# Optimization experiments

Hardware: AMD Instinct MI355X
Metric: run time of the kernel (lower is better)

## Reference

```python
import jax, jax.numpy as jnp
import numpy as np


def _pairwise_sq_dist(x, y):
    # x: [B, N, 3], y: [B, M, 3] -> P: [B, N, M] squared Euclidean distances
    xx = jnp.sum(x * x, axis=-1)                      # [B, N]
    yy = jnp.sum(y * y, axis=-1)                      # [B, M]
    zz = jnp.einsum('bnd,bmd->bnm', x, y)             # [B, N, M]
    return xx[:, :, None] + yy[:, None, :] - 2.0 * zz


def setup_inputs() -> dict:
    key = jax.random.key(0)
    k1, k2 = jax.random.split(key)
    B, K = 8, 8192
    adv_pc = jax.random.normal(k1, (B, K, 3), dtype=jnp.float32)
    ori_pc = jax.random.normal(k2, (B, K, 3), dtype=jnp.float32)
    weights = jnp.ones((B,), dtype=jnp.float32)
    return {"adv_pc": adv_pc, "ori_pc": ori_pc, "weights": weights}


def reference(adv_pc, ori_pc, weights):
    # P = pairwise_dist(gts=ori_pc, preds=adv_pc): [B, N_ori, N_adv]
    P = _pairwise_sq_dist(ori_pc, adv_pc)
    # method='adv2ori': loss1 = max over adv points of min over ori points
    loss1 = jnp.max(jnp.min(P, axis=1), axis=1)       # [B]
    loss = loss1 * weights
    return jnp.mean(loss)                             # batch_avg=True
```

## Files before the change

### kernel.cpp

```cpp
#include <hip/hip_runtime.h>


#define KPTS 8192
#define BATCH 8
#define NSPLIT 8
#define RBLK (KPTS / NSPLIT)
#define TSLICE (RBLK / 32)
#define CBLK 512
#define MCHUNK (KPTS / CBLK)
#define AHALF_B (KPTS * 16)

typedef _Float16 half8 __attribute__((ext_vector_type(8)));
typedef float f32x16 __attribute__((ext_vector_type(16)));

__device__ __forceinline__ float min16acc(float rm, const f32x16 c) {
    float u0 = fminf(fminf(c[0],  c[1]),  c[2]);
    float u1 = fminf(fminf(c[3],  c[4]),  c[5]);
    float u2 = fminf(fminf(c[6],  c[7]),  c[8]);
    float u3 = fminf(fminf(c[9],  c[10]), c[11]);
    float u4 = fminf(fminf(c[12], c[13]), c[14]);
    float u5 = fminf(fminf(u0, u1), c[15]);
    float u6 = fminf(fminf(u2, u3), u4);
    return fminf(fminf(u5, u6), rm);
}

__global__ __launch_bounds__(256) void prep(const float* __restrict__ ori,
                                            _Float16* __restrict__ Ap) {
    const int g = blockIdx.x * 256 + threadIdx.x;
    const int b = g >> 13;
    const int n = g & (KPTS - 1);

    const float* op = ori + (size_t)g * 3;
    float x = op[0], y = op[1], z = op[2];
    float oo = x * x + y * y + z * z;
    const _Float16 Z = (_Float16)0.0f;
    _Float16 hx = (_Float16)x, hy = (_Float16)y, hz = (_Float16)z;
    _Float16 lx = (_Float16)(x - (float)hx);
    _Float16 ly = (_Float16)(y - (float)hy);
    _Float16 lz = (_Float16)(z - (float)hz);
    _Float16 oh = (_Float16)oo;
    _Float16 ol = (_Float16)(oo - (float)oh);
    half8 a0 = {hx, hy, hz, hx, hy, hz, lx, ly};
    half8 a1 = {lz, oh, ol, Z, Z, Z, Z, Z};

    _Float16* base = Ap + (size_t)b * AHALF_B + ((n >> 5) << 9) + ((n & 31) << 3);
    *(half8*)base         = a0;
    *(half8*)(base + 256) = a1;
}

__global__ __launch_bounds__(256) void hausdorff(const float* __restrict__ adv,
                                                 const _Float16* __restrict__ Ap,
                                                 float* __restrict__ part,
                                                 float* __restrict__ out) {
    const int bid  = blockIdx.x;
    const int b    = bid >> 7;
    const int mc   = (bid >> 3) & (MCHUNK - 1);
    const int ns   = bid & 7;
    const int tid  = threadIdx.x;
    const int lane = tid & 63;
    const int wv   = tid >> 6;
    const int r    = lane & 31;
    const int hk   = lane >> 5;

    if (bid == 0 && tid == 0) out[0] = 0.0f;

    const _Float16 Z = (_Float16)0.0f, ONE = (_Float16)1.0f;

    const float* advb = adv + (size_t)b * KPTS * 3;
    const int m0 = mc * CBLK + wv * 128 + r;
    half8 bf0, bf1, bf2, bf3;
    float aa0, aa1, aa2, aa3;
#pragma unroll
    for (int i = 0; i < 4; ++i) {
        const int m = m0 + 32 * i;
        float ax = advb[3 * m], ay = advb[3 * m + 1], az = advb[3 * m + 2];
        float aa = ax * ax + ay * ay + az * az;
        float tx = -2.f * ax, ty = -2.f * ay, tz = -2.f * az;
        _Float16 bx = (_Float16)tx, by = (_Float16)ty, bz = (_Float16)tz;
        _Float16 cx = (_Float16)(tx - (float)bx);
        _Float16 cy = (_Float16)(ty - (float)by);
        _Float16 cz = (_Float16)(tz - (float)bz);
        half8 h0 = {bx, by, bz, cx, cy, cz, bx, by};
        half8 h1 = {bz, ONE, ONE, Z, Z, Z, Z, Z};
        half8 bi = hk ? h1 : h0;
        if (i == 0) { bf0 = bi; aa0 = aa; }
        else if (i == 1) { bf1 = bi; aa1 = aa; }
        else if (i == 2) { bf2 = bi; aa2 = aa; }
        else { bf3 = bi; aa3 = aa; }
    }

    f32x16 zc;
#pragma unroll
    for (int i = 0; i < 16; ++i) zc[i] = 0.0f;

    float rm0 = __builtin_huge_valf(), rm1 = __builtin_huge_valf();
    float rm2 = __builtin_huge_valf(), rm3 = __builtin_huge_valf();

    const half8* __restrict__ ap =
        (const half8*)(Ap + (size_t)b * AHALF_B + (size_t)ns * TSLICE * 512) + lane;

    half8 af = ap[0];
#pragma unroll 4
    for (int t = 0; t < TSLICE; ++t) {
        half8 afn = ap[(t + 1) * 64];
        f32x16 c0 = __builtin_amdgcn_mfma_f32_32x32x16_f16(af, bf0, zc, 0, 0, 0);
        f32x16 c1 = __builtin_amdgcn_mfma_f32_32x32x16_f16(af, bf1, zc, 0, 0, 0);
        f32x16 c2 = __builtin_amdgcn_mfma_f32_32x32x16_f16(af, bf2, zc, 0, 0, 0);
        f32x16 c3 = __builtin_amdgcn_mfma_f32_32x32x16_f16(af, bf3, zc, 0, 0, 0);
        rm0 = min16acc(rm0, c0);
        rm1 = min16acc(rm1, c1);
        rm2 = min16acc(rm2, c2);
        rm3 = min16acc(rm3, c3);
        af = afn;
    }

    rm0 = fminf(rm0, __shfl_xor(rm0, 32, 64));
    rm1 = fminf(rm1, __shfl_xor(rm1, 32, 64));
    rm2 = fminf(rm2, __shfl_xor(rm2, 32, 64));
    rm3 = fminf(rm3, __shfl_xor(rm3, 32, 64));

    float* p = part + ((size_t)ns * BATCH + b) * KPTS;
    if (hk == 0) {
        p[m0]      = fmaxf(rm0 + aa0, 0.0f);
        p[m0 + 32] = fmaxf(rm1 + aa1, 0.0f);
        p[m0 + 64] = fmaxf(rm2 + aa2, 0.0f);
        p[m0 + 96] = fmaxf(rm3 + aa3, 0.0f);
    }
}

__global__ __launch_bounds__(1024) void reduceB(const float* __restrict__ part,
                                                const float* __restrict__ w,
                                                float* __restrict__ out) {
    const int b = blockIdx.x;
    const int tid = threadIdx.x;

    float mx = 0.0f;
#pragma unroll
    for (int h = 0; h < 2; ++h) {
        const int c4 = tid + h * 1024;
        float4 v[NSPLIT];
#pragma unroll
        for (int s = 0; s < NSPLIT; ++s)
            v[s] = *(const float4*)(part + ((size_t)s * BATCH + b) * KPTS + (size_t)c4 * 4);
        float4 mn = v[0];
#pragma unroll
        for (int s = 1; s < NSPLIT; ++s) {
            mn.x = fminf(mn.x, v[s].x); mn.y = fminf(mn.y, v[s].y);
            mn.z = fminf(mn.z, v[s].z); mn.w = fminf(mn.w, v[s].w);
        }
        mx = fmaxf(mx, fmaxf(fmaxf(mn.x, mn.y), fmaxf(mn.z, mn.w)));
    }

#pragma unroll
    for (int off = 32; off; off >>= 1)
        mx = fmaxf(mx, __shfl_xor(mx, off, 64));

    __shared__ float red[16];
    if ((tid & 63) == 0) red[tid >> 6] = mx;
    __syncthreads();
    if (tid == 0) {
        float m2 = red[0];
#pragma unroll
        for (int i = 1; i < 16; ++i) m2 = fmaxf(m2, red[i]);
        atomicAdd(out, m2 * w[b] * (1.0f / BATCH));
    }
}

extern "C" void kernel_launch(void* const* d_in, const int* in_sizes, int n_in,
                              void* d_out, int out_size, void* d_ws, size_t ws_size,
                              hipStream_t stream) {
    const float* adv = (const float*)d_in[0];
    const float* ori = (const float*)d_in[1];
    const float* w   = (const float*)d_in[2];
    float* out = (float*)d_out;

    char* ws = (char*)d_ws;
    _Float16* Ap = (_Float16*)ws;
    float* part = (float*)(ws + (size_t)(2 << 20) + 4096);

    prep<<<(BATCH * KPTS) / 256, 256, 0, stream>>>(ori, Ap);
    hausdorff<<<BATCH * MCHUNK * NSPLIT, 256, 0, stream>>>(adv, (const _Float16*)Ap, part, out);
    reduceB<<<BATCH, 1024, 0, stream>>>((const float*)part, w, out);
}
```

Measured before the change: 89.17 us.

## Fuse ori-point preprocessing into hausdorff kernel via LDS staging and inline-asm MFMA

Drops the separate prep kernel. Each block now converts its slice of ori points into split-fp16 MFMA operands itself and stages them in shared memory, then reads A fragments from LDS instead of global memory. The four MFMAs are issued through inline asm followed by fixed s_nop padding, and the unroll pragma is removed. This saves one launch and the global round trip, but every block repeats the conversion (16x redundant across column chunks), adds a barrier, and hard-codes nops that may stall the pipeline.

```diff
diff --git a/kernel.cpp b/kernel.cpp
--- a/kernel.cpp
+++ b/kernel.cpp
@@ -8,7 +8,6 @@
 #define TSLICE (RBLK / 32)
 #define CBLK 512
 #define MCHUNK (KPTS / CBLK)
-#define AHALF_B (KPTS * 16)
 
 typedef _Float16 half8 __attribute__((ext_vector_type(8)));
 typedef float f32x16 __attribute__((ext_vector_type(16)));
@@ -24,34 +23,12 @@
     return fminf(fminf(u5, u6), rm);
 }
 
-__global__ __launch_bounds__(256) void prep(const float* __restrict__ ori,
-                                            _Float16* __restrict__ Ap) {
-    const int g = blockIdx.x * 256 + threadIdx.x;
-    const int b = g >> 13;
-    const int n = g & (KPTS - 1);
-
-    const float* op = ori + (size_t)g * 3;
-    float x = op[0], y = op[1], z = op[2];
-    float oo = x * x + y * y + z * z;
-    const _Float16 Z = (_Float16)0.0f;
-    _Float16 hx = (_Float16)x, hy = (_Float16)y, hz = (_Float16)z;
-    _Float16 lx = (_Float16)(x - (float)hx);
-    _Float16 ly = (_Float16)(y - (float)hy);
-    _Float16 lz = (_Float16)(z - (float)hz);
-    _Float16 oh = (_Float16)oo;
-    _Float16 ol = (_Float16)(oo - (float)oh);
-    half8 a0 = {hx, hy, hz, hx, hy, hz, lx, ly};
-    half8 a1 = {lz, oh, ol, Z, Z, Z, Z, Z};
-
-    _Float16* base = Ap + (size_t)b * AHALF_B + ((n >> 5) << 9) + ((n & 31) << 3);
-    *(half8*)base         = a0;
-    *(half8*)(base + 256) = a1;
-}
-
 __global__ __launch_bounds__(256) void hausdorff(const float* __restrict__ adv,
-                                                 const _Float16* __restrict__ Ap,
+                                                 const float* __restrict__ ori,
                                                  float* __restrict__ part,
                                                  float* __restrict__ out) {
+    __shared__ _Float16 sA[(TSLICE + 1) * 512];
+
     const int bid  = blockIdx.x;
     const int b    = bid >> 7;
     const int mc   = (bid >> 3) & (MCHUNK - 1);
@@ -89,6 +66,27 @@
         else { bf3 = bi; aa3 = aa; }
     }
 
+    const float* orib = ori + ((size_t)b * KPTS + (size_t)ns * RBLK) * 3;
+#pragma unroll
+    for (int i = 0; i < 4; ++i) {
+        const int rr = tid + i * 256;
+        const float* op = orib + (size_t)rr * 3;
+        float x = op[0], y = op[1], z = op[2];
+        float oo = x * x + y * y + z * z;
+        _Float16 hx = (_Float16)x, hy = (_Float16)y, hz = (_Float16)z;
+        _Float16 lx = (_Float16)(x - (float)hx);
+        _Float16 ly = (_Float16)(y - (float)hy);
+        _Float16 lz = (_Float16)(z - (float)hz);
+        _Float16 oh = (_Float16)oo;
+        _Float16 ol = (_Float16)(oo - (float)oh);
+        half8 a0 = {hx, hy, hz, hx, hy, hz, lx, ly};
+        half8 a1 = {lz, oh, ol, Z, Z, Z, Z, Z};
+        const int off = ((rr >> 5) << 9) + ((rr & 31) << 3);
+        *(half8*)(&sA[off])       = a0;
+        *(half8*)(&sA[off + 256]) = a1;
+    }
+    __syncthreads();
+
     f32x16 zc;
 #pragma unroll
     for (int i = 0; i < 16; ++i) zc[i] = 0.0f;
@@ -96,21 +94,25 @@
     float rm0 = __builtin_huge_valf(), rm1 = __builtin_huge_valf();
     float rm2 = __builtin_huge_valf(), rm3 = __builtin_huge_valf();
 
-    const half8* __restrict__ ap =
-        (const half8*)(Ap + (size_t)b * AHALF_B + (size_t)ns * TSLICE * 512) + lane;
+    const _Float16* apl = sA + lane * 8;
+    half8 af = *(const half8*)apl;
 
-    half8 af = ap[0];
-#pragma unroll 4
     for (int t = 0; t < TSLICE; ++t) {
-        half8 afn = ap[(t + 1) * 64];
-        f32x16 c0 = __builtin_amdgcn_mfma_f32_32x32x16_f16(af, bf0, zc, 0, 0, 0);
-        f32x16 c1 = __builtin_amdgcn_mfma_f32_32x32x16_f16(af, bf1, zc, 0, 0, 0);
-        f32x16 c2 = __builtin_amdgcn_mfma_f32_32x32x16_f16(af, bf2, zc, 0, 0, 0);
-        f32x16 c3 = __builtin_amdgcn_mfma_f32_32x32x16_f16(af, bf3, zc, 0, 0, 0);
-        rm0 = min16acc(rm0, c0);
-        rm1 = min16acc(rm1, c1);
-        rm2 = min16acc(rm2, c2);
-        rm3 = min16acc(rm3, c3);
+        half8 afn = *(const half8*)(apl + (size_t)(t + 1) * 512);
+
+        f32x16 d0, d1, d2, d3;
+        asm("v_mfma_f32_32x32x16_f16 %0, %4, %5, %9\n\t"
+            "v_mfma_f32_32x32x16_f16 %1, %4, %6, %9\n\t"
+            "v_mfma_f32_32x32x16_f16 %2, %4, %7, %9\n\t"
+            "v_mfma_f32_32x32x16_f16 %3, %4, %8, %9\n\t"
+            "s_nop 7\n\ts_nop 7\n\ts_nop 7\n\ts_nop 7"
+            : "=&v"(d0), "=&v"(d1), "=&v"(d2), "=&v"(d3)
+            : "v"(af), "v"(bf0), "v"(bf1), "v"(bf2), "v"(bf3), "v"(zc));
+
+        rm0 = min16acc(rm0, d0);
+        rm1 = min16acc(rm1, d1);
+        rm2 = min16acc(rm2, d2);
+        rm3 = min16acc(rm3, d3);
         af = afn;
     }
 
@@ -173,12 +175,8 @@
     const float* ori = (const float*)d_in[1];
     const float* w   = (const float*)d_in[2];
     float* out = (float*)d_out;
+    float* part = (float*)d_ws;
 
-    char* ws = (char*)d_ws;
-    _Float16* Ap = (_Float16*)ws;
-    float* part = (float*)(ws + (size_t)(2 << 20) + 4096);
-
-    prep<<<(BATCH * KPTS) / 256, 256, 0, stream>>>(ori, Ap);
-    hausdorff<<<BATCH * MCHUNK * NSPLIT, 256, 0, stream>>>(adv, (const _Float16*)Ap, part, out);
+    hausdorff<<<BATCH * MCHUNK * NSPLIT, 256, 0, stream>>>(adv, ori, part, out);
     reduceB<<<BATCH, 1024, 0, stream>>>((const float*)part, w, out);
 }
```

New measurement: 78.69 us. 1.13x faster.
